# Performance work log

Measured on AMD Instinct MI355X. Metric: run time of the kernel, lower is better.

The kernel has to match this reference:

```python
import jax, jax.numpy as jnp
import numpy as np

IM_SIZE = (256, 256)
OVERSAMP = 1.25
WIDTH = 6
BETA = float(np.pi * np.sqrt((WIDTH / OVERSAMP * (OVERSAMP - 0.5)) ** 2 - 0.8))
OS_SIZE = tuple(int(np.ceil(OVERSAMP * n)) for n in IM_SIZE)  # (320, 320)
D = 2


def _kb(x):
    # Kaiser-Bessel interpolation kernel: i0(beta*sqrt(1-x^2)) for |x|<=1 (sigpy convention)
    return jnp.i0(BETA * jnp.sqrt(jnp.maximum(1.0 - x * x, 0.0)))


def setup_inputs() -> dict:
    key = jax.random.key(0)
    k1, k2, k3 = jax.random.split(key, 3)
    N, C = 1, 8
    img_r = jax.random.normal(k1, (N, C) + IM_SIZE, dtype=jnp.float32)
    img_i = jax.random.normal(k2, (N, C) + IM_SIZE, dtype=jnp.float32)
    # trajectory in [-N_i/2, N_i/2] per the class docstring
    trj = (jax.random.uniform(k3, (N, 64, 4096, D), dtype=jnp.float32) - 0.5) * 256.0
    return {"img_r": img_r, "img_i": img_i, "trj": trj}


def _nufft_forward(img_r, img_i, trj):
    img = (img_r + 1j * img_i).astype(jnp.complex64)  # (N, C, H, W)
    nd = img.ndim
    # --- apodization (inverse FT of KB kernel), separable per axis ---
    for a in range(D):
        n, osn = IM_SIZE[a], OS_SIZE[a]
        idx = jnp.arange(n, dtype=jnp.float32)
        arg = jnp.sqrt(BETA ** 2 - (np.pi * WIDTH * (idx - n // 2) / osn) ** 2)
        apod = arg / jnp.sinh(arg)
        shape = [1] * nd
        shape[nd - D + a] = n
        img = img * apod.reshape(shape)
    # --- scale + centered zero-pad to oversampled grid ---
    img = img / np.sqrt(float(np.prod(IM_SIZE)))
    pads = [(0, 0)] * (nd - D) + [(((o - n) // 2), (o - n) - ((o - n) // 2))
                                  for n, o in zip(IM_SIZE, OS_SIZE)]
    img = jnp.pad(img, pads)
    # --- centered FFT (ifftshift -> fftn(norm=None) -> fftshift) ---
    axes = tuple(range(-D, 0))
    ksp_os = jnp.fft.fftshift(jnp.fft.fftn(jnp.fft.ifftshift(img, axes=axes), axes=axes), axes=axes)
    # --- scale trajectory to oversampled grid coordinates ---
    scale = jnp.array([OS_SIZE[a] / IM_SIZE[a] for a in range(D)], jnp.float32)
    shift = jnp.array([OS_SIZE[a] // 2 for a in range(D)], jnp.float32)
    coord = trj * scale + shift  # (N, R, S, 2)
    x0 = jnp.ceil(coord - WIDTH / 2.0)
    # --- KB interpolation: fixed 6x6 neighbor loop, vectorized gather over all points ---
    N = img.shape[0]
    out = jnp.zeros((N,) + img.shape[1:nd - D] + coord.shape[1:-1], jnp.complex64)

    def gather(grid, ix, iy):  # grid (C, Hos, Wos), ix/iy (R, S) -> (C, R, S)
        return grid[:, ix, iy]

    for dx in range(WIDTH):
        px = x0[..., 0] + dx
        wx = _kb((px - coord[..., 0]) / (WIDTH / 2.0))
        ix = px.astype(jnp.int32) % OS_SIZE[0]
        for dy in range(WIDTH):
            py = x0[..., 1] + dy
            wy = _kb((py - coord[..., 1]) / (WIDTH / 2.0))
            iy = py.astype(jnp.int32) % OS_SIZE[1]
            vals = jax.vmap(gather)(ksp_os, ix, iy)  # (N, C, R, S)
            out = out + vals * (wx * wy)[:, None, :, :]
    return out / (WIDTH ** D)


def reference(img_r, img_i, trj):
    return _nufft_forward(img_r, img_i, trj)
```

## Files before the change

### kernel.cpp

```cpp
#include <hip/hip_runtime.h>
#include <math.h>

#define NCH   8
#define IMN   256
#define OSN   320
#define NPTS  (64*4096)
#define KD    512
#define BETA_F   10.9551078f
#define BETA2_F  120.014389f
#define APOD_C   0.05890486225f
#define GROWS 326
#define GCOLS 328
#define GPITCH (GCOLS * NCH)

typedef unsigned short u16;
typedef unsigned int   u32;
typedef __attribute__((ext_vector_type(8))) short s16x8;
typedef __attribute__((ext_vector_type(4))) float f32x4;
typedef __attribute__((ext_vector_type(2))) float f32x2;

__device__ __forceinline__ u32 f2bf(float f) {
    u32 u = __float_as_uint(f);
    return (u + 0x7FFFu + ((u >> 16) & 1u)) >> 16;
}

__device__ __forceinline__ s16x8 derive_b2(s16x8 b) {
    union { s16x8 v; u32 d[4]; } in, out;
    in.v = b;
    #pragma unroll
    for (int i = 0; i < 4; i++) {
        u32 v = in.d[i];
        out.d[i] = ((v >> 16) | (v << 16)) ^ 0x8000u;
    }
    return out.v;
}

__device__ __forceinline__ float i0f(float t) {
    if (t < 3.75f) {
        float y = t * t * (1.0f / 14.0625f);
        return 1.0f + y * (3.5156229f + y * (3.0899424f + y * (1.2067492f +
                     y * (0.2659732f + y * (0.0360768f + y * 0.0045813f)))));
    }
    float z = 3.75f / t;
    float p = 0.39894228f + z * (0.01328592f + z * (0.00225319f + z * (-0.00157565f +
              z * (0.00916281f + z * (-0.02057706f + z * (0.02635537f +
              z * (-0.01647633f + z * 0.00392377f)))))));
    return expf(t) * rsqrtf(t) * p;
}

__device__ __forceinline__ float apodf(int i) {
    float x = APOD_C * (float)(i - IMN / 2);
    float arg = sqrtf(BETA2_F - x * x);
    float e = expf(arg);
    float sh = 0.5f * (e - 1.0f / e);
    return arg / sh;
}

__global__ void prep(const float* __restrict__ r, const float* __restrict__ im,
                     u32* __restrict__ B1, u32* __restrict__ A) {
    const int b = blockIdx.x, t = threadIdx.x;
    if (b < (OSN * IMN) / 256) {
        int idx = b * 256 + t;
        int k = idx >> 8, j = idx & 255;
        int p = (k * (j + 32)) % OSN;
        float th = (2.0f * (float)M_PI / (float)OSN) * (float)p;
        float s = ((k + j) & 1) ? -1.0f : 1.0f;
        float sn, cs;
        sincosf(th, &sn, &cs);
        float re = s * cs, imv = -s * sn;
        B1[idx] = f2bf(re) | (f2bf(-imv) << 16);
    } else {
        int idx = (b - (OSN * IMN) / 256) * 256 + t;
        int i2 = idx & 255, i1 = (idx >> 8) & 255;
        float w = apodf(i1) * apodf(i2) * (1.0f / 256.0f);
        A[idx] = f2bf(r[idx] * w) | (f2bf(im[idx] * w) << 16);
    }
}

__launch_bounds__(64)
__global__ void gemm1(const short* __restrict__ Abf, const short* __restrict__ B1,
                      short* __restrict__ Tb) {
    const int c = blockIdx.z;
    const int mBase = blockIdx.y * 32;
    const int nBase = blockIdx.x * 16;
    const int t = threadIdx.x;
    const int fm = t & 15, fq = (t >> 4) * 8;
    const short* pa0  = Abf + (long)(c * IMN + mBase + fm) * KD + fq;
    const short* pa1  = pa0 + 16 * KD;
    const short* pb10 = B1 + (long)(nBase + fm) * KD + fq;
    f32x4 zz = {0.f, 0.f, 0.f, 0.f};
    f32x4 accRe[2], accIm[2];
    #pragma unroll
    for (int i = 0; i < 2; i++) { accRe[i] = zz; accIm[i] = zz; }

    #pragma unroll
    for (int kc = 0; kc < 16; kc++) {
        const int kb = kc * 32;
        s16x8 a0  = *(const s16x8*)(pa0  + kb);
        s16x8 a1  = *(const s16x8*)(pa1  + kb);
        s16x8 b10 = *(const s16x8*)(pb10 + kb);
        s16x8 b20 = derive_b2(b10);
        accRe[0] = __builtin_amdgcn_mfma_f32_16x16x32_bf16(a0, b10, accRe[0], 0, 0, 0);
        accRe[1] = __builtin_amdgcn_mfma_f32_16x16x32_bf16(a1, b10, accRe[1], 0, 0, 0);
        accIm[0] = __builtin_amdgcn_mfma_f32_16x16x32_bf16(a0, b20, accIm[0], 0, 0, 0);
        accIm[1] = __builtin_amdgcn_mfma_f32_16x16x32_bf16(a1, b20, accIm[1], 0, 0, 0);
    }
    #pragma unroll
    for (int i = 0; i < 2; i++) {
        int i1b = mBase + i * 16 + (t >> 4) * 4;
        int k2  = nBase + fm;
        s16x8 v;
        #pragma unroll
        for (int r = 0; r < 4; r++) {
            v[2 * r]     = (short)f2bf(accRe[i][r]);
            v[2 * r + 1] = (short)f2bf(accIm[i][r]);
        }
        *(s16x8*)(Tb + ((long)(c * OSN + k2)) * KD + 2 * i1b) = v;
    }
}

__launch_bounds__(64)
__global__ void gemm2(const short* __restrict__ B1, const short* __restrict__ Tb,
                      u32* __restrict__ Gb) {
    const int c = blockIdx.z;
    const int mBase = blockIdx.y * 32;
    const int nBase = blockIdx.x * 16;
    const int t = threadIdx.x;
    const int fm = t & 15, fq = (t >> 4) * 8;
    const short* pa10 = B1 + (long)(mBase + fm) * KD + fq;
    const short* pa11 = pa10 + 16 * KD;
    const short* pb0  = Tb + ((long)(c * OSN + nBase + fm)) * KD + fq;
    f32x4 zz = {0.f, 0.f, 0.f, 0.f};
    f32x4 accRe[2], accIm[2];
    #pragma unroll
    for (int i = 0; i < 2; i++) { accRe[i] = zz; accIm[i] = zz; }

    #pragma unroll
    for (int kc = 0; kc < 16; kc++) {
        const int kb = kc * 32;
        s16x8 a10 = *(const s16x8*)(pa10 + kb);
        s16x8 a11 = *(const s16x8*)(pa11 + kb);
        s16x8 b0  = *(const s16x8*)(pb0  + kb);
        s16x8 a20 = derive_b2(a10);
        s16x8 a21 = derive_b2(a11);
        accRe[0] = __builtin_amdgcn_mfma_f32_16x16x32_bf16(a10, b0, accRe[0], 0, 0, 0);
        accRe[1] = __builtin_amdgcn_mfma_f32_16x16x32_bf16(a11, b0, accRe[1], 0, 0, 0);
        accIm[0] = __builtin_amdgcn_mfma_f32_16x16x32_bf16(a20, b0, accIm[0], 0, 0, 0);
        accIm[1] = __builtin_amdgcn_mfma_f32_16x16x32_bf16(a21, b0, accIm[1], 0, 0, 0);
    }
    #pragma unroll
    for (int i = 0; i < 2; i++) {
        int k2 = nBase + fm;
        int pc  = k2 + 3;
        int pc2 = (k2 < 3) ? (k2 + 323) : ((k2 >= 317) ? (k2 - 317) : -1);
        #pragma unroll
        for (int r = 0; r < 4; r++) {
            int k1 = mBase + i * 16 + (t >> 4) * 4 + r;
            u32 val = f2bf(accRe[i][r]) | (f2bf(accIm[i][r]) << 16);
            int pr  = k1 + 3;
            int pr2 = (k1 < 3) ? (k1 + 323) : ((k1 >= 317) ? (k1 - 317) : -1);
            Gb[(long)pr * GPITCH + pc * NCH + c] = val;
            if (pr2 >= 0)              Gb[(long)pr2 * GPITCH + pc  * NCH + c] = val;
            if (pc2 >= 0)              Gb[(long)pr  * GPITCH + pc2 * NCH + c] = val;
            if (pr2 >= 0 && pc2 >= 0)  Gb[(long)pr2 * GPITCH + pc2 * NCH + c] = val;
        }
    }
}

__launch_bounds__(256, 4)
__global__ void interp_kernel(const float* __restrict__ trj,
                              const u32* __restrict__ grid,
                              u32* __restrict__ out) {
    const int t = threadIdx.x;
    __shared__ float wxs[64][6], wys[64][6];
    __shared__ int   x0s[64], y0s[64];

    #pragma unroll
    for (int k = 0; k < 3; k++) {
        int e = t + 256 * k;
        int ptl = e / 12;
        int rem = e - ptl * 12;
        int axis = rem >= 6 ? 1 : 0;
        int d = rem - axis * 6;
        int pt = blockIdx.x * 64 + ptl;
        float tv = trj[pt * 2 + axis];
        float cc = __fadd_rn(__fmul_rn(tv, 1.25f), 160.0f);
        float v0 = ceilf(__fadd_rn(cc, -3.0f));
        if (d == 0) {
            if (axis) y0s[ptl] = (int)v0; else x0s[ptl] = (int)v0;
        }
        float u = __fdiv_rn(__fsub_rn(v0 + (float)d, cc), 3.0f);
        float wv = i0f(BETA_F * sqrtf(fmaxf(1.0f - u * u, 0.0f)));
        if (axis) wys[ptl][d] = wv; else wxs[ptl][d] = wv;
    }
    __syncthreads();

    const int pl = t >> 2;
    const int cp = (t & 3) * 2;
    const int px = x0s[pl] + 3;
    const int py = y0s[pl] + 3;
    const u32* g0 = grid + (long)px * GPITCH + py * NCH + cp;

    uint2 g[36];
    #pragma unroll
    for (int dx = 0; dx < 6; dx++)
        #pragma unroll
        for (int dy = 0; dy < 6; dy++)
            g[dx * 6 + dy] = *(const uint2*)(g0 + dx * GPITCH + dy * NCH);

    float wx[6], wy[6];
    #pragma unroll
    for (int d = 0; d < 6; d++) { wx[d] = wxs[pl][d]; wy[d] = wys[pl][d]; }

    f32x2 a0 = {0.f, 0.f}, a1 = {0.f, 0.f};
    #pragma unroll
    for (int dx = 0; dx < 6; dx++) {
        float wxv = wx[dx];
        #pragma unroll
        for (int dy = 0; dy < 6; dy++) {
            uint2 gv = g[dx * 6 + dy];
            float ww = wxv * wy[dy];
            f32x2 w2 = {ww, ww};
            f32x2 v0v = { __uint_as_float(gv.x << 16), __uint_as_float(gv.x & 0xFFFF0000u) };
            f32x2 v1v = { __uint_as_float(gv.y << 16), __uint_as_float(gv.y & 0xFFFF0000u) };
            a0 += v0v * w2;
            a1 += v1v * w2;
        }
    }
    f32x2 sc = {1.0f / 36.0f, 1.0f / 36.0f};
    a0 *= sc; a1 *= sc;

    __shared__ float2 lds[64][9];
    lds[pl][cp]     = make_float2(a0.x, a0.y);
    lds[pl][cp + 1] = make_float2(a1.x, a1.y);
    __syncthreads();
    int c2 = t >> 5, p2 = t & 31;
    float2 va = lds[p2][c2];
    float2 vb = lds[p2 + 32][c2];
    long ob = (long)c2 * NPTS + blockIdx.x * 64;
    out[ob + p2]      = f2bf(va.y) | (f2bf(va.x) << 16);
    out[ob + p2 + 32] = f2bf(vb.y) | (f2bf(vb.x) << 16);
}

extern "C" void kernel_launch(void* const* d_in, const int* in_sizes, int n_in,
                              void* d_out, int out_size, void* d_ws, size_t ws_size,
                              hipStream_t stream) {
    const float* img_r = (const float*)d_in[0];
    const float* img_i = (const float*)d_in[1];
    const float* trj   = (const float*)d_in[2];

    char* ob = (char*)d_out;
    short* Tb  = (short*)(ob);
    u32*  B1u  = (u32*)(ob + 2621440);
    u32*  Au   = (u32*)(ob + 3276800);
    u32*  Gb   = (u32*)d_ws;

    prep<<<(OSN * IMN) / 256 + (NCH * IMN * IMN) / 256, 256, 0, stream>>>(
        img_r, img_i, B1u, Au);
    gemm1<<<dim3(OSN / 16, IMN / 32, NCH), 64, 0, stream>>>(
        (const short*)Au, (const short*)B1u, Tb);
    gemm2<<<dim3(OSN / 16, OSN / 32, NCH), 64, 0, stream>>>(
        (const short*)B1u, Tb, Gb);
    interp_kernel<<<NPTS / 64, 256, 0, stream>>>(trj, Gb, (u32*)d_out);
}
```

Before: 109.0 us.

## Fuse prep, two GEMMs and interpolation into one cooperative persistent kernel

```diff
diff --git a/kernel.cpp b/kernel.cpp
--- a/kernel.cpp
+++ b/kernel.cpp
@@ -1,5 +1,8 @@
 #include <hip/hip_runtime.h>
+#include <hip/hip_cooperative_groups.h>
 #include <math.h>
+
+namespace cg = cooperative_groups;
 
 #define NCH   8
 #define IMN   256
@@ -56,190 +59,195 @@
     return arg / sh;
 }
 
-__global__ void prep(const float* __restrict__ r, const float* __restrict__ im,
-                     u32* __restrict__ B1, u32* __restrict__ A) {
-    const int b = blockIdx.x, t = threadIdx.x;
-    if (b < (OSN * IMN) / 256) {
-        int idx = b * 256 + t;
-        int k = idx >> 8, j = idx & 255;
-        int p = (k * (j + 32)) % OSN;
-        float th = (2.0f * (float)M_PI / (float)OSN) * (float)p;
-        float s = ((k + j) & 1) ? -1.0f : 1.0f;
-        float sn, cs;
-        sincosf(th, &sn, &cs);
-        float re = s * cs, imv = -s * sn;
-        B1[idx] = f2bf(re) | (f2bf(-imv) << 16);
-    } else {
-        int idx = (b - (OSN * IMN) / 256) * 256 + t;
-        int i2 = idx & 255, i1 = (idx >> 8) & 255;
-        float w = apodf(i1) * apodf(i2) * (1.0f / 256.0f);
-        A[idx] = f2bf(r[idx] * w) | (f2bf(im[idx] * w) << 16);
-    }
-}
-
-__launch_bounds__(64)
-__global__ void gemm1(const short* __restrict__ Abf, const short* __restrict__ B1,
-                      short* __restrict__ Tb) {
-    const int c = blockIdx.z;
-    const int mBase = blockIdx.y * 32;
-    const int nBase = blockIdx.x * 16;
+__launch_bounds__(256, 4)
+__global__ void fused(const float* __restrict__ img_r, const float* __restrict__ img_i,
+                      const float* __restrict__ trj,
+                      u32* __restrict__ B1, u32* __restrict__ A,
+                      short* __restrict__ Tb, u32* __restrict__ Gb,
+                      u32* __restrict__ out) {
+    cg::grid_group gg = cg::this_grid();
     const int t = threadIdx.x;
-    const int fm = t & 15, fq = (t >> 4) * 8;
-    const short* pa0  = Abf + (long)(c * IMN + mBase + fm) * KD + fq;
-    const short* pa1  = pa0 + 16 * KD;
-    const short* pb10 = B1 + (long)(nBase + fm) * KD + fq;
-    f32x4 zz = {0.f, 0.f, 0.f, 0.f};
-    f32x4 accRe[2], accIm[2];
-    #pragma unroll
-    for (int i = 0; i < 2; i++) { accRe[i] = zz; accIm[i] = zz; }
-
-    #pragma unroll
-    for (int kc = 0; kc < 16; kc++) {
-        const int kb = kc * 32;
-        s16x8 a0  = *(const s16x8*)(pa0  + kb);
-        s16x8 a1  = *(const s16x8*)(pa1  + kb);
-        s16x8 b10 = *(const s16x8*)(pb10 + kb);
-        s16x8 b20 = derive_b2(b10);
-        accRe[0] = __builtin_amdgcn_mfma_f32_16x16x32_bf16(a0, b10, accRe[0], 0, 0, 0);
-        accRe[1] = __builtin_amdgcn_mfma_f32_16x16x32_bf16(a1, b10, accRe[1], 0, 0, 0);
-        accIm[0] = __builtin_amdgcn_mfma_f32_16x16x32_bf16(a0, b20, accIm[0], 0, 0, 0);
-        accIm[1] = __builtin_amdgcn_mfma_f32_16x16x32_bf16(a1, b20, accIm[1], 0, 0, 0);
-    }
-    #pragma unroll
-    for (int i = 0; i < 2; i++) {
-        int i1b = mBase + i * 16 + (t >> 4) * 4;
-        int k2  = nBase + fm;
-        s16x8 v;
-        #pragma unroll
-        for (int r = 0; r < 4; r++) {
-            v[2 * r]     = (short)f2bf(accRe[i][r]);
-            v[2 * r + 1] = (short)f2bf(accIm[i][r]);
-        }
-        *(s16x8*)(Tb + ((long)(c * OSN + k2)) * KD + 2 * i1b) = v;
-    }
-}
-
-__launch_bounds__(64)
-__global__ void gemm2(const short* __restrict__ B1, const short* __restrict__ Tb,
-                      u32* __restrict__ Gb) {
-    const int c = blockIdx.z;
-    const int mBase = blockIdx.y * 32;
-    const int nBase = blockIdx.x * 16;
-    const int t = threadIdx.x;
-    const int fm = t & 15, fq = (t >> 4) * 8;
-    const short* pa10 = B1 + (long)(mBase + fm) * KD + fq;
-    const short* pa11 = pa10 + 16 * KD;
-    const short* pb0  = Tb + ((long)(c * OSN + nBase + fm)) * KD + fq;
-    f32x4 zz = {0.f, 0.f, 0.f, 0.f};
-    f32x4 accRe[2], accIm[2];
-    #pragma unroll
-    for (int i = 0; i < 2; i++) { accRe[i] = zz; accIm[i] = zz; }
-
-    #pragma unroll
-    for (int kc = 0; kc < 16; kc++) {
-        const int kb = kc * 32;
-        s16x8 a10 = *(const s16x8*)(pa10 + kb);
-        s16x8 a11 = *(const s16x8*)(pa11 + kb);
-        s16x8 b0  = *(const s16x8*)(pb0  + kb);
-        s16x8 a20 = derive_b2(a10);
-        s16x8 a21 = derive_b2(a11);
-        accRe[0] = __builtin_amdgcn_mfma_f32_16x16x32_bf16(a10, b0, accRe[0], 0, 0, 0);
-        accRe[1] = __builtin_amdgcn_mfma_f32_16x16x32_bf16(a11, b0, accRe[1], 0, 0, 0);
-        accIm[0] = __builtin_amdgcn_mfma_f32_16x16x32_bf16(a20, b0, accIm[0], 0, 0, 0);
-        accIm[1] = __builtin_amdgcn_mfma_f32_16x16x32_bf16(a21, b0, accIm[1], 0, 0, 0);
-    }
-    #pragma unroll
-    for (int i = 0; i < 2; i++) {
-        int k2 = nBase + fm;
-        int pc  = k2 + 3;
-        int pc2 = (k2 < 3) ? (k2 + 323) : ((k2 >= 317) ? (k2 - 317) : -1);
-        #pragma unroll
-        for (int r = 0; r < 4; r++) {
-            int k1 = mBase + i * 16 + (t >> 4) * 4 + r;
-            u32 val = f2bf(accRe[i][r]) | (f2bf(accIm[i][r]) << 16);
-            int pr  = k1 + 3;
-            int pr2 = (k1 < 3) ? (k1 + 323) : ((k1 >= 317) ? (k1 - 317) : -1);
-            Gb[(long)pr * GPITCH + pc * NCH + c] = val;
-            if (pr2 >= 0)              Gb[(long)pr2 * GPITCH + pc  * NCH + c] = val;
-            if (pc2 >= 0)              Gb[(long)pr  * GPITCH + pc2 * NCH + c] = val;
-            if (pr2 >= 0 && pc2 >= 0)  Gb[(long)pr2 * GPITCH + pc2 * NCH + c] = val;
-        }
-    }
-}
-
-__launch_bounds__(256, 4)
-__global__ void interp_kernel(const float* __restrict__ trj,
-                              const u32* __restrict__ grid,
-                              u32* __restrict__ out) {
-    const int t = threadIdx.x;
+    const int nb = gridDim.x;
+    const int nwaves = nb * 4;
+    const int wid0 = blockIdx.x * 4 + (t >> 6);
+    const int lt = t & 63;
+
+    for (int b = blockIdx.x; b < (OSN * IMN) / 256 + (NCH * IMN * IMN) / 256; b += nb) {
+        if (b < (OSN * IMN) / 256) {
+            int idx = b * 256 + t;
+            int k = idx >> 8, j = idx & 255;
+            int p = (k * (j + 32)) % OSN;
+            float th = (2.0f * (float)M_PI / (float)OSN) * (float)p;
+            float s = ((k + j) & 1) ? -1.0f : 1.0f;
+            float sn, cs;
+            sincosf(th, &sn, &cs);
+            float re = s * cs, imv = -s * sn;
+            B1[idx] = f2bf(re) | (f2bf(-imv) << 16);
+        } else {
+            int idx = (b - (OSN * IMN) / 256) * 256 + t;
+            int i2 = idx & 255, i1 = (idx >> 8) & 255;
+            float w = apodf(i1) * apodf(i2) * (1.0f / 256.0f);
+            A[idx] = f2bf(img_r[idx] * w) | (f2bf(img_i[idx] * w) << 16);
+        }
+    }
+    gg.sync();
+
+    for (int w = wid0; w < 1280; w += nwaves) {
+        const int nx = w % 20, my = (w / 20) % 8, c = w / 160;
+        const int mBase = my * 32;
+        const int nBase = nx * 16;
+        const int fm = lt & 15, fq = (lt >> 4) * 8;
+        const short* Abf = (const short*)A;
+        const short* B1s_ = (const short*)B1;
+        const short* pa0  = Abf + (long)(c * IMN + mBase + fm) * KD + fq;
+        const short* pa1  = pa0 + 16 * KD;
+        const short* pb10 = B1s_ + (long)(nBase + fm) * KD + fq;
+        f32x4 zz = {0.f, 0.f, 0.f, 0.f};
+        f32x4 accRe[2], accIm[2];
+        #pragma unroll
+        for (int i = 0; i < 2; i++) { accRe[i] = zz; accIm[i] = zz; }
+        #pragma unroll
+        for (int kc = 0; kc < 16; kc++) {
+            const int kb = kc * 32;
+            s16x8 a0  = *(const s16x8*)(pa0  + kb);
+            s16x8 a1  = *(const s16x8*)(pa1  + kb);
+            s16x8 b10 = *(const s16x8*)(pb10 + kb);
+            s16x8 b20 = derive_b2(b10);
+            accRe[0] = __builtin_amdgcn_mfma_f32_16x16x32_bf16(a0, b10, accRe[0], 0, 0, 0);
+            accRe[1] = __builtin_amdgcn_mfma_f32_16x16x32_bf16(a1, b10, accRe[1], 0, 0, 0);
+            accIm[0] = __builtin_amdgcn_mfma_f32_16x16x32_bf16(a0, b20, accIm[0], 0, 0, 0);
+            accIm[1] = __builtin_amdgcn_mfma_f32_16x16x32_bf16(a1, b20, accIm[1], 0, 0, 0);
+        }
+        #pragma unroll
+        for (int i = 0; i < 2; i++) {
+            int i1b = mBase + i * 16 + (lt >> 4) * 4;
+            int k2  = nBase + fm;
+            s16x8 v;
+            #pragma unroll
+            for (int r = 0; r < 4; r++) {
+                v[2 * r]     = (short)f2bf(accRe[i][r]);
+                v[2 * r + 1] = (short)f2bf(accIm[i][r]);
+            }
+            *(s16x8*)(Tb + ((long)(c * OSN + k2)) * KD + 2 * i1b) = v;
+        }
+    }
+    gg.sync();
+
+    for (int w = wid0; w < 1600; w += nwaves) {
+        const int nx = w % 20, my = (w / 20) % 10, c = w / 200;
+        const int mBase = my * 32;
+        const int nBase = nx * 16;
+        const int fm = lt & 15, fq = (lt >> 4) * 8;
+        const short* B1s_ = (const short*)B1;
+        const short* pa10 = B1s_ + (long)(mBase + fm) * KD + fq;
+        const short* pa11 = pa10 + 16 * KD;
+        const short* pb0  = Tb + ((long)(c * OSN + nBase + fm)) * KD + fq;
+        f32x4 zz = {0.f, 0.f, 0.f, 0.f};
+        f32x4 accRe[2], accIm[2];
+        #pragma unroll
+        for (int i = 0; i < 2; i++) { accRe[i] = zz; accIm[i] = zz; }
+        #pragma unroll
+        for (int kc = 0; kc < 16; kc++) {
+            const int kb = kc * 32;
+            s16x8 a10 = *(const s16x8*)(pa10 + kb);
+            s16x8 a11 = *(const s16x8*)(pa11 + kb);
+            s16x8 b0  = *(const s16x8*)(pb0  + kb);
+            s16x8 a20 = derive_b2(a10);
+            s16x8 a21 = derive_b2(a11);
+            accRe[0] = __builtin_amdgcn_mfma_f32_16x16x32_bf16(a10, b0, accRe[0], 0, 0, 0);
+            accRe[1] = __builtin_amdgcn_mfma_f32_16x16x32_bf16(a11, b0, accRe[1], 0, 0, 0);
+            accIm[0] = __builtin_amdgcn_mfma_f32_16x16x32_bf16(a20, b0, accIm[0], 0, 0, 0);
+            accIm[1] = __builtin_amdgcn_mfma_f32_16x16x32_bf16(a21, b0, accIm[1], 0, 0, 0);
+        }
+        #pragma unroll
+        for (int i = 0; i < 2; i++) {
+            int k2 = nBase + fm;
+            int pc  = k2 + 3;
+            int pc2 = (k2 < 3) ? (k2 + 323) : ((k2 >= 317) ? (k2 - 317) : -1);
+            #pragma unroll
+            for (int r = 0; r < 4; r++) {
+                int k1 = mBase + i * 16 + (lt >> 4) * 4 + r;
+                u32 val = f2bf(accRe[i][r]) | (f2bf(accIm[i][r]) << 16);
+                int pr  = k1 + 3;
+                int pr2 = (k1 < 3) ? (k1 + 323) : ((k1 >= 317) ? (k1 - 317) : -1);
+                Gb[(long)pr * GPITCH + pc * NCH + c] = val;
+                if (pr2 >= 0)              Gb[(long)pr2 * GPITCH + pc  * NCH + c] = val;
+                if (pc2 >= 0)              Gb[(long)pr  * GPITCH + pc2 * NCH + c] = val;
+                if (pr2 >= 0 && pc2 >= 0)  Gb[(long)pr2 * GPITCH + pc2 * NCH + c] = val;
+            }
+        }
+    }
+    gg.sync();
+
     __shared__ float wxs[64][6], wys[64][6];
     __shared__ int   x0s[64], y0s[64];
-
-    #pragma unroll
-    for (int k = 0; k < 3; k++) {
-        int e = t + 256 * k;
-        int ptl = e / 12;
-        int rem = e - ptl * 12;
-        int axis = rem >= 6 ? 1 : 0;
-        int d = rem - axis * 6;
-        int pt = blockIdx.x * 64 + ptl;
-        float tv = trj[pt * 2 + axis];
-        float cc = __fadd_rn(__fmul_rn(tv, 1.25f), 160.0f);
-        float v0 = ceilf(__fadd_rn(cc, -3.0f));
-        if (d == 0) {
-            if (axis) y0s[ptl] = (int)v0; else x0s[ptl] = (int)v0;
-        }
-        float u = __fdiv_rn(__fsub_rn(v0 + (float)d, cc), 3.0f);
-        float wv = i0f(BETA_F * sqrtf(fmaxf(1.0f - u * u, 0.0f)));
-        if (axis) wys[ptl][d] = wv; else wxs[ptl][d] = wv;
-    }
-    __syncthreads();
-
-    const int pl = t >> 2;
-    const int cp = (t & 3) * 2;
-    const int px = x0s[pl] + 3;
-    const int py = y0s[pl] + 3;
-    const u32* g0 = grid + (long)px * GPITCH + py * NCH + cp;
-
-    uint2 g[36];
-    #pragma unroll
-    for (int dx = 0; dx < 6; dx++)
-        #pragma unroll
-        for (int dy = 0; dy < 6; dy++)
-            g[dx * 6 + dy] = *(const uint2*)(g0 + dx * GPITCH + dy * NCH);
-
-    float wx[6], wy[6];
-    #pragma unroll
-    for (int d = 0; d < 6; d++) { wx[d] = wxs[pl][d]; wy[d] = wys[pl][d]; }
-
-    f32x2 a0 = {0.f, 0.f}, a1 = {0.f, 0.f};
-    #pragma unroll
-    for (int dx = 0; dx < 6; dx++) {
-        float wxv = wx[dx];
-        #pragma unroll
-        for (int dy = 0; dy < 6; dy++) {
-            uint2 gv = g[dx * 6 + dy];
-            float ww = wxv * wy[dy];
-            f32x2 w2 = {ww, ww};
-            f32x2 v0v = { __uint_as_float(gv.x << 16), __uint_as_float(gv.x & 0xFFFF0000u) };
-            f32x2 v1v = { __uint_as_float(gv.y << 16), __uint_as_float(gv.y & 0xFFFF0000u) };
-            a0 += v0v * w2;
-            a1 += v1v * w2;
-        }
-    }
-    f32x2 sc = {1.0f / 36.0f, 1.0f / 36.0f};
-    a0 *= sc; a1 *= sc;
-
-    __shared__ float2 lds[64][9];
-    lds[pl][cp]     = make_float2(a0.x, a0.y);
-    lds[pl][cp + 1] = make_float2(a1.x, a1.y);
-    __syncthreads();
-    int c2 = t >> 5, p2 = t & 31;
-    float2 va = lds[p2][c2];
-    float2 vb = lds[p2 + 32][c2];
-    long ob = (long)c2 * NPTS + blockIdx.x * 64;
-    out[ob + p2]      = f2bf(va.y) | (f2bf(va.x) << 16);
-    out[ob + p2 + 32] = f2bf(vb.y) | (f2bf(vb.x) << 16);
+    __shared__ float2 ldsr[64][9];
+    for (int b = blockIdx.x; b < NPTS / 64; b += nb) {
+        #pragma unroll
+        for (int k = 0; k < 3; k++) {
+            int e = t + 256 * k;
+            int ptl = e / 12;
+            int rem = e - ptl * 12;
+            int axis = rem >= 6 ? 1 : 0;
+            int d = rem - axis * 6;
+            int pt = b * 64 + ptl;
+            float tv = trj[pt * 2 + axis];
+            float cc = __fadd_rn(__fmul_rn(tv, 1.25f), 160.0f);
+            float v0 = ceilf(__fadd_rn(cc, -3.0f));
+            if (d == 0) {
+                if (axis) y0s[ptl] = (int)v0; else x0s[ptl] = (int)v0;
+            }
+            float u = __fdiv_rn(__fsub_rn(v0 + (float)d, cc), 3.0f);
+            float wv = i0f(BETA_F * sqrtf(fmaxf(1.0f - u * u, 0.0f)));
+            if (axis) wys[ptl][d] = wv; else wxs[ptl][d] = wv;
+        }
+        __syncthreads();
+
+        const int pl = t >> 2;
+        const int cp = (t & 3) * 2;
+        const int px = x0s[pl] + 3;
+        const int py = y0s[pl] + 3;
+        const u32* g0 = Gb + (long)px * GPITCH + py * NCH + cp;
+
+        uint2 g[36];
+        #pragma unroll
+        for (int dx = 0; dx < 6; dx++)
+            #pragma unroll
+            for (int dy = 0; dy < 6; dy++)
+                g[dx * 6 + dy] = *(const uint2*)(g0 + dx * GPITCH + dy * NCH);
+
+        float wx[6], wy[6];
+        #pragma unroll
+        for (int d = 0; d < 6; d++) { wx[d] = wxs[pl][d]; wy[d] = wys[pl][d]; }
+
+        f32x2 a0 = {0.f, 0.f}, a1 = {0.f, 0.f};
+        #pragma unroll
+        for (int dx = 0; dx < 6; dx++) {
+            float wxv = wx[dx];
+            #pragma unroll
+            for (int dy = 0; dy < 6; dy++) {
+                uint2 gv = g[dx * 6 + dy];
+                float ww = wxv * wy[dy];
+                f32x2 w2 = {ww, ww};
+                f32x2 v0v = { __uint_as_float(gv.x << 16), __uint_as_float(gv.x & 0xFFFF0000u) };
+                f32x2 v1v = { __uint_as_float(gv.y << 16), __uint_as_float(gv.y & 0xFFFF0000u) };
+                a0 += v0v * w2;
+                a1 += v1v * w2;
+            }
+        }
+        f32x2 sc = {1.0f / 36.0f, 1.0f / 36.0f};
+        a0 *= sc; a1 *= sc;
+
+        ldsr[pl][cp]     = make_float2(a0.x, a0.y);
+        ldsr[pl][cp + 1] = make_float2(a1.x, a1.y);
+        __syncthreads();
+        int c2 = t >> 5, p2 = t & 31;
+        float2 va = ldsr[p2][c2];
+        float2 vb = ldsr[p2 + 32][c2];
+        long obase = (long)c2 * NPTS + b * 64;
+        out[obase + p2]      = f2bf(va.y) | (f2bf(va.x) << 16);
+        out[obase + p2 + 32] = f2bf(vb.y) | (f2bf(vb.x) << 16);
+    }
 }
 
 extern "C" void kernel_launch(void* const* d_in, const int* in_sizes, int n_in,
@@ -254,12 +262,19 @@
     u32*  B1u  = (u32*)(ob + 2621440);
     u32*  Au   = (u32*)(ob + 3276800);
     u32*  Gb   = (u32*)d_ws;
-
-    prep<<<(OSN * IMN) / 256 + (NCH * IMN * IMN) / 256, 256, 0, stream>>>(
-        img_r, img_i, B1u, Au);
-    gemm1<<<dim3(OSN / 16, IMN / 32, NCH), 64, 0, stream>>>(
-        (const short*)Au, (const short*)B1u, Tb);
-    gemm2<<<dim3(OSN / 16, OSN / 32, NCH), 64, 0, stream>>>(
-        (const short*)B1u, Tb, Gb);
-    interp_kernel<<<NPTS / 64, 256, 0, stream>>>(trj, Gb, (u32*)d_out);
-}
+    u32*  outp = (u32*)d_out;
+
+    static int nblk = -1;
+    if (nblk < 0) {
+        if (hipOccupancyMaxActiveBlocksPerMultiprocessor(&nblk, fused, 256, 0)
+                != hipSuccess || nblk < 1)
+            nblk = 2;
+    }
+    int grid = nblk * 256;
+    if (grid > 4096) grid = 4096;
+
+    void* args[] = { (void*)&img_r, (void*)&img_i, (void*)&trj,
+                     (void*)&B1u, (void*)&Au, (void*)&Tb, (void*)&Gb,
+                     (void*)&outp };
+    hipLaunchCooperativeKernel((void*)fused, dim3(grid), dim3(256), args, 0, stream);
+}
```

Measured after the change: 285.7 us. 162% more time.
